# Performance work log

Measured on AMD Instinct MI355X. Metric: run time of the kernel, lower is better.

Reference implementation:

```python
import jax, jax.numpy as jnp
import numpy as np

# --- config (matches init_kwargs) ---
HID = 2048      # hidden_size
H = 16          # num_attention_heads
D_NOPE = 128    # qk_nope_head_dim
D_ROPE = 64     # qk_rope_head_dim
D_Q = D_NOPE + D_ROPE  # 192
D_V = 128       # v_head_dim
QR = 1536       # q_lora_rank
KVR = 512       # kv_lora_rank
PH = 16         # pattern_heads
PD = HID // PH  # 128
THETA = 10000.0
EPS = 1e-6


def rmsnorm(x, w):
    var = jnp.mean(jnp.square(x), axis=-1, keepdims=True)
    return x * jax.lax.rsqrt(var + EPS) * w


def rope_cos_sin(seq_len):
    inv_freq = 1.0 / (THETA ** (jnp.arange(0, D_ROPE, 2, dtype=jnp.float32) / D_ROPE))
    t = jnp.arange(seq_len, dtype=jnp.float32)
    freqs = jnp.outer(t, inv_freq)            # [S, D_ROPE/2]
    emb = jnp.concatenate([freqs, freqs], -1)  # [S, D_ROPE]
    return jnp.cos(emb), jnp.sin(emb)


def rotate_half(x):
    x1, x2 = jnp.split(x, 2, axis=-1)
    return jnp.concatenate([-x2, x1], axis=-1)


def apply_rope(x, cos, sin):
    # x: [B, H, S, D_ROPE]; cos/sin: [S, D_ROPE]
    return x * cos[None, None] + rotate_half(x) * sin[None, None]


def setup_inputs() -> dict:
    key = jax.random.key(0)
    ks = jax.random.split(key, 12)
    def w(k, shape):
        return (jax.random.normal(k, shape, jnp.float32) / np.sqrt(shape[-1])).astype(jnp.float32)
    B, S = 2, 1024
    return {
        "hidden_states": jax.random.normal(ks[0], (B, S, HID), jnp.float32),
        "q_a_w": w(ks[1], (QR, HID)),
        "q_a_ln_w": jnp.ones((QR,), jnp.float32),
        "q_b_w": w(ks[2], (H * D_Q, QR)),
        "kv_a_w": w(ks[3], (KVR + H * D_ROPE, HID)),
        "kv_a_ln_w": jnp.ones((KVR,), jnp.float32),
        "kv_b_w": w(ks[4], (H * (D_NOPE + D_V), KVR)),
        "o_w": w(ks[5], (HID, H * D_V)),
        "sp_q_w": w(ks[6], (HID, HID)),
        "sp_k_w": w(ks[7], (HID, HID)),
        "sp_v_w": w(ks[8], (HID, HID)),
        "sp_o_w": w(ks[9], (HID, HID)),
        "gate_w": w(ks[10], (2, HID)),
        "gate_b": jnp.zeros((2,), jnp.float32),
    }


def reference(hidden_states, q_a_w, q_a_ln_w, q_b_w, kv_a_w, kv_a_ln_w, kv_b_w,
              o_w, sp_q_w, sp_k_w, sp_v_w, sp_o_w, gate_w, gate_b):
    b, s, _ = hidden_states.shape
    dt = hidden_states.dtype

    # ---- main MLA path ----
    q_mid = rmsnorm(hidden_states @ q_a_w.T, q_a_ln_w)                      # [B,S,QR]
    q = (q_mid @ q_b_w.T).reshape(b, s, H, D_Q).transpose(0, 2, 1, 3)       # [B,H,S,Dq]
    q_nope, q_pe = q[..., :D_NOPE], q[..., D_NOPE:]

    kv_a = hidden_states @ kv_a_w.T                                         # [B,S,KVR+H*Dr]
    kv_lora, k_pe_flat = kv_a[..., :KVR], kv_a[..., KVR:]
    k_pe = k_pe_flat.reshape(b, s, H, D_ROPE).transpose(0, 2, 1, 3)         # [B,H,S,Dr]

    kv = (rmsnorm(kv_lora, kv_a_ln_w) @ kv_b_w.T)
    kv = kv.reshape(b, s, H, D_NOPE + D_V).transpose(0, 2, 1, 3)            # [B,H,S,Dn+Dv]
    k_nope, v = kv[..., :D_NOPE], kv[..., D_NOPE:]

    cos, sin = rope_cos_sin(s)
    q_pe = apply_rope(q_pe, cos, sin)
    k_pe = apply_rope(k_pe, cos, sin)

    qf = jnp.concatenate([q_nope, q_pe], -1)                                # [B,H,S,Dq]
    kf = jnp.concatenate([k_nope, k_pe], -1)

    scale = D_Q ** -0.5
    scores = jnp.einsum('bhqd,bhkd->bhqk', qf, kf) * scale
    probs = jax.nn.softmax(scores.astype(jnp.float32), axis=-1).astype(dt)
    ctx = jnp.einsum('bhqk,bhkd->bhqd', probs, v)                           # [B,H,S,Dv]
    main_out = ctx.transpose(0, 2, 1, 3).reshape(b, s, H * D_V) @ o_w.T     # [B,S,HID]

    # ---- self pattern path (standard MHA on hidden_states) ----
    def split_heads(x):
        return x.reshape(b, s, PH, PD).transpose(0, 2, 1, 3)
    pq = split_heads(hidden_states @ sp_q_w.T)
    pk = split_heads(hidden_states @ sp_k_w.T)
    pv = split_heads(hidden_states @ sp_v_w.T)
    p_scores = jnp.einsum('bhqd,bhkd->bhqk', pq, pk) * (PD ** -0.5)
    p_probs = jax.nn.softmax(p_scores.astype(jnp.float32), axis=-1).astype(dt)
    p_ctx = jnp.einsum('bhqk,bhkd->bhqd', p_probs, pv)
    pattern_out = p_ctx.transpose(0, 2, 1, 3).reshape(b, s, HID) @ sp_o_w.T

    # ---- learned gate over paths ----
    gates = jax.nn.softmax(hidden_states @ gate_w.T + gate_b, axis=-1)      # [B,S,2]
    return gates[..., 0:1] * main_out + gates[..., 1:2] * pattern_out
```

## Files before the change

kernel.cpp:

```cpp
#include <hip/hip_runtime.h>
#include <math.h>
#include <stdint.h>

#define HIDN  2048
#define NH    16
#define DNOPE 128
#define DROPE 64
#define DQ    192
#define DV    128
#define QRANK 1536
#define KVRANK 512
#define SEQ   1024
#define NBATCH 2
#define NTOK  (NBATCH*SEQ)
#define EPSV  1e-6f

typedef unsigned short u16;
typedef unsigned int   u32;
typedef __attribute__((ext_vector_type(8))) short  short8;
typedef __attribute__((ext_vector_type(8))) unsigned short ushort8;
typedef __attribute__((ext_vector_type(4))) float  f32x4;

__device__ __forceinline__ u16 f2b(float f) {
    u32 u = __float_as_uint(f);
    u = (u + 0x7fffu + ((u >> 16) & 1u)) >> 16;
    return (u16)u;
}
__device__ __forceinline__ float b2f(u16 h) {
    return __uint_as_float(((u32)h) << 16);
}

__device__ __forceinline__ void async_copy16(const u16* g, u16* l) {
    __builtin_amdgcn_global_load_lds(
        (const __attribute__((address_space(1))) u32*)g,
        (__attribute__((address_space(3))) u32*)l,
        16, 0, 0);
}

__device__ __forceinline__ int swz(int r, int c) { return r * 4 + (c ^ ((r >> 1) & 3)); }

struct CastArgs {
    const float* s[10];
    u16* d[10];
    int cum[11];
};
__global__ __launch_bounds__(256)
void cast_all(CastArgs a, int total_chunks)
{
    int c = blockIdx.x * 256 + threadIdx.x;
    if (c >= total_chunks) return;
    int seg = 0;
    #pragma unroll
    for (int i = 1; i < 10; ++i) seg += (c >= a.cum[i]) ? 1 : 0;
    int local = c - a.cum[seg];
    const float* src = a.s[seg] + (size_t)local * 8;
    u16* dst = a.d[seg] + (size_t)local * 8;
    float4 x = *(const float4*)(src);
    float4 y = *(const float4*)(src + 4);
    ushort8 o;
    o[0]=f2b(x.x); o[1]=f2b(x.y); o[2]=f2b(x.z); o[3]=f2b(x.w);
    o[4]=f2b(y.x); o[5]=f2b(y.y); o[6]=f2b(y.z); o[7]=f2b(y.w);
    *(ushort8*)(dst) = o;
}

struct GemmSeg {
    const u16* X; const u16* W;
    float* Cf; u16* Cb; u16* Cb2; u16* Cb3;
    int K; int ldx; int ldc; int mode; int bx0;
};
struct GemmArgs { GemmSeg seg[3]; int nseg; };

__global__ __launch_bounds__(256)
void gemm_multi(GemmArgs a)
{
    __shared__ __align__(16) u16 As[2 * 4096];
    __shared__ __align__(16) u16 Bs[2 * 4096];
    int s = 0;
    if (a.nseg > 1 && (int)blockIdx.x >= a.seg[1].bx0) s = 1;
    if (a.nseg > 2 && (int)blockIdx.x >= a.seg[2].bx0) s = 2;
    const GemmSeg g = a.seg[s];

    const int tid = threadIdx.x;
    const int bn = ((int)blockIdx.x - g.bx0) * 128;
    const int bm = blockIdx.y * 128;
    const int lane = tid & 63, wv = tid >> 6;
    const int lm = lane & 15, lq = lane >> 4;
    const int wm = (wv >> 1) * 64, wn = (wv & 1) * 64;
    const int ldx = g.ldx, K = g.K;
    const u16* Xp = g.X;
    const u16* Wp = g.W;

    auto stage = [&](int kt, int buf) {
        int k0 = kt * 32;
        #pragma unroll
        for (int it = 0; it < 2; ++it) {
            int base = wv * 64 + it * 256;
            int slot = base + lane;
            int r = slot >> 2, c = (slot & 3) ^ ((r >> 1) & 3);
            async_copy16(Xp + (size_t)(bm + r) * ldx + k0 + c * 8,
                         As + buf * 4096 + base * 8);
            async_copy16(Wp + (size_t)(bn + r) * K + k0 + c * 8,
                         Bs + buf * 4096 + base * 8);
        }
    };

    f32x4 acc[4][4] = {};
    const int niter = K >> 5;
    stage(0, 0);
    for (int kt = 0; kt < niter; ++kt) {
        int cur = kt & 1;
        __syncthreads();
        if (kt + 1 < niter) stage(kt + 1, cur ^ 1);
        const u16* Ab = As + cur * 4096;
        const u16* Bb = Bs + cur * 4096;
        short8 af[4], bf[4];
        #pragma unroll
        for (int mt = 0; mt < 4; ++mt) {
            int R = wm + mt * 16 + lm;
            af[mt] = *(const short8*)(Ab + swz(R, lq) * 8);
        }
        #pragma unroll
        for (int nt = 0; nt < 4; ++nt) {
            int R = wn + nt * 16 + lm;
            bf[nt] = *(const short8*)(Bb + swz(R, lq) * 8);
        }
        #pragma unroll
        for (int mt = 0; mt < 4; ++mt)
            #pragma unroll
            for (int nt = 0; nt < 4; ++nt)
                acc[mt][nt] = __builtin_amdgcn_mfma_f32_16x16x32_bf16(
                    af[mt], bf[nt], acc[mt][nt], 0, 0, 0);
    }

    const int mode = g.mode;
    #pragma unroll
    for (int mt = 0; mt < 4; ++mt) {
        int token0 = bm + wm + mt * 16 + lq * 4;
        #pragma unroll
        for (int nt = 0; nt < 4; ++nt) {
            int feat = bn + wn + nt * 16 + lm;
            #pragma unroll
            for (int i = 0; i < 4; ++i) {
                float v = acc[mt][nt][i];
                int tok = token0 + i;
                int b2 = tok >> 10, s2 = tok & (SEQ - 1);
                if (mode == 0) {
                    g.Cf[(size_t)tok * g.ldc + feat] = v;
                } else if (mode == 5) {
                    g.Cb[(size_t)tok * g.ldc + feat] = f2b(v);
                } else if (mode == 1) {
                    int h2 = feat / DQ, d = feat - h2 * DQ;
                    g.Cb[((size_t)((b2 * NH + h2) * SEQ + s2)) * DQ + d] = f2b(v);
                } else if (mode == 3) {
                    int h2 = feat >> 8, c = feat & 255;
                    if (c < 128)
                        g.Cb[((size_t)((b2 * NH + h2) * SEQ + s2)) * DQ + c] = f2b(v);
                    else
                        g.Cb2[((size_t)((b2 * NH + h2) * 128 + (c - 128))) * SEQ + s2] = f2b(v);
                } else {
                    int wsel = feat >> 11;
                    int f2 = feat & 2047;
                    int h2 = f2 >> 7, d = f2 & 127;
                    if (wsel == 0)
                        g.Cb[((size_t)((b2 * NH + h2) * SEQ + s2)) * 128 + d] = f2b(v);
                    else if (wsel == 1)
                        g.Cb2[((size_t)((b2 * NH + h2) * SEQ + s2)) * 128 + d] = f2b(v);
                    else
                        g.Cb3[((size_t)((b2 * NH + h2) * 128 + d)) * SEQ + s2] = f2b(v);
                }
            }
        }
    }
}

__global__ __launch_bounds__(256)
void rmsnorm_fused(u16* __restrict__ amid, const float* __restrict__ qw,
                   const float* __restrict__ kvw)
{
    int row = blockIdx.x;
    u16* x; const float* w; int D;
    if (row < NTOK) { x = amid + (size_t)row * 3072;            w = qw;  D = QRANK; }
    else            { x = amid + (size_t)(row - NTOK) * 3072 + QRANK; w = kvw; D = KVRANK; }
    float ss = 0.f;
    for (int d = threadIdx.x; d < D; d += 256) { float v = b2f(x[d]); ss += v * v; }
    __shared__ float red[256];
    red[threadIdx.x] = ss;
    __syncthreads();
    for (int off = 128; off > 0; off >>= 1) {
        if (threadIdx.x < off) red[threadIdx.x] += red[threadIdx.x + off];
        __syncthreads();
    }
    float inv = rsqrtf(red[0] / (float)D + EPSV);
    for (int d = threadIdx.x; d < D; d += 256)
        x[d] = f2b(b2f(x[d]) * inv * w[d]);
}

__global__ __launch_bounds__(256)
void rope_fused(u16* __restrict__ qf, const u16* __restrict__ amid,
                u16* __restrict__ kf)
{
    int t = blockIdx.x * 256 + threadIdx.x;
    bool isq = t < (1 << 20);
    int tt = isq ? t : t - (1 << 20);
    int i = tt & 31, s = (tt >> 5) & (SEQ - 1), bh = tt >> 15;
    float inv_freq = exp2f((float)i * -0.41524101186f);
    float ang = (float)s * inv_freq;
    float c, sn; sincosf(ang, &sn, &c);
    if (isq) {
        u16* p = qf + ((size_t)bh * SEQ + s) * DQ;
        float x1 = b2f(p[DNOPE + i]), x2 = b2f(p[DNOPE + 32 + i]);
        p[DNOPE + i]      = f2b(x1 * c - x2 * sn);
        p[DNOPE + 32 + i] = f2b(x2 * c + x1 * sn);
    } else {
        int h = bh & (NH - 1), bb = bh >> 4;
        const u16* src = amid + ((size_t)(bb * SEQ + s)) * 3072 + (QRANK + KVRANK) + h * DROPE;
        float x1 = b2f(src[i]), x2 = b2f(src[32 + i]);
        u16* dst = kf + ((size_t)bh * SEQ + s) * DQ + DNOPE;
        dst[i]      = f2b(x1 * c - x2 * sn);
        dst[32 + i] = f2b(x2 * c + x1 * sn);
    }
}

template<int DQK>
__device__ __forceinline__
void flash_body(const u16* __restrict__ Q, const u16* __restrict__ Kf,
                const u16* __restrict__ Vt, u16* __restrict__ ctx_out,
                float scale, u16* Ks, u16* Vs, u16* Ps, int qt, int h, int bb)
{
    constexpr int KSZ  = 32 * DQK;
    constexpr int VSZ  = 32 * 128;
    constexpr int NKIT = DQK / 64;
    constexpr int NT   = SEQ / 32;
    const int tid = threadIdx.x, lane = tid & 63, wv = tid >> 6;
    const int lm = lane & 15, lq = lane >> 4;
    const size_t bh = (size_t)bb * NH + h;
    const u16* Qb = Q + (bh * SEQ + qt * 64 + wv * 16) * (size_t)DQK;
    const u16* Kb = Kf + bh * SEQ * (size_t)DQK;
    const u16* Vb = Vt + bh * (size_t)128 * SEQ;

    short8 qfrag[DQK / 32];
    #pragma unroll
    for (int ks = 0; ks < DQK / 32; ++ks)
        qfrag[ks] = *(const short8*)(Qb + lm * DQK + ks * 32 + lq * 8);

    auto stage = [&](int kt, int buf) {
        #pragma unroll
        for (int it = 0; it < NKIT; ++it) {
            int base = it * 256 + wv * 64;
            int slot = base + lane;
            int plane = slot >> 7, rem = slot & 127;
            int key = rem >> 2, c = (rem & 3) ^ ((key >> 1) & 3);
            async_copy16(Kb + (size_t)(kt * 32 + key) * DQK + plane * 32 + c * 8,
                         Ks + buf * KSZ + base * 8);
        }
        #pragma unroll
        for (int it = 0; it < 2; ++it) {
            int base = it * 256 + wv * 64;
            int slot = base + lane;
            int d = slot >> 2, c = (slot & 3) ^ ((d >> 1) & 3);
            async_copy16(Vb + (size_t)d * SEQ + kt * 32 + c * 8,
                         Vs + buf * VSZ + base * 8);
        }
    };

    float m_i[4], l_i[4];
    #pragma unroll
    for (int i = 0; i < 4; ++i) { m_i[i] = -INFINITY; l_i[i] = 0.f; }
    f32x4 oacc[8] = {};

    stage(0, 0);
    for (int kt = 0; kt < NT; ++kt) {
        int cur = kt & 1;
        __syncthreads();
        if (kt + 1 < NT) stage(kt + 1, cur ^ 1);
        const u16* Kc = Ks + cur * KSZ;
        const u16* Vc = Vs + cur * VSZ;

        f32x4 sacc[2] = {};
        __builtin_amdgcn_s_setprio(1);
        #pragma unroll
        for (int kb = 0; kb < 2; ++kb)
            #pragma unroll
            for (int ks = 0; ks < DQK / 32; ++ks) {
                int R = kb * 16 + lm;
                short8 kfr = *(const short8*)(Kc + ks * 1024 + swz(R, lq) * 8);
                sacc[kb] = __builtin_amdgcn_mfma_f32_16x16x32_bf16(
                    qfrag[ks], kfr, sacc[kb], 0, 0, 0);
            }
        __builtin_amdgcn_s_setprio(0);

        float s0v[4], s1v[4], mx[4];
        #pragma unroll
        for (int i = 0; i < 4; ++i) {
            float s0 = sacc[0][i] * scale, s1 = sacc[1][i] * scale;
            float m2 = fmaxf(s0, s1);
            m2 = fmaxf(m2, __shfl_xor(m2, 1));
            m2 = fmaxf(m2, __shfl_xor(m2, 2));
            m2 = fmaxf(m2, __shfl_xor(m2, 4));
            m2 = fmaxf(m2, __shfl_xor(m2, 8));
            s0v[i] = s0; s1v[i] = s1; mx[i] = m2;
        }
        bool need = false;
        #pragma unroll
        for (int i = 0; i < 4; ++i) need |= (mx[i] > m_i[i] + 8.f);
        need = __any(need);
        float alpha[4];
        if (need) {
            #pragma unroll
            for (int i = 0; i < 4; ++i) {
                float mnew = fmaxf(m_i[i], mx[i]);
                alpha[i] = __expf(m_i[i] - mnew);
                m_i[i] = mnew;
                l_i[i] *= alpha[i];
            }
        }
        float p0[4], p1[4];
        #pragma unroll
        for (int i = 0; i < 4; ++i) {
            p0[i] = __expf(s0v[i] - m_i[i]);
            p1[i] = __expf(s1v[i] - m_i[i]);
            float sum = p0[i] + p1[i];
            sum += __shfl_xor(sum, 1);
            sum += __shfl_xor(sum, 2);
            sum += __shfl_xor(sum, 4);
            sum += __shfl_xor(sum, 8);
            l_i[i] += sum;
        }

        u16* Pw = Ps + wv * 640;
        #pragma unroll
        for (int i = 0; i < 4; ++i) {
            Pw[(lq * 4 + i) * 40 + lm]      = f2b(p0[i]);
            Pw[(lq * 4 + i) * 40 + 16 + lm] = f2b(p1[i]);
        }
        short8 pfrag = *(const short8*)(Pw + lm * 40 + lq * 8);

        if (need) {
            #pragma unroll
            for (int nt = 0; nt < 8; ++nt)
                #pragma unroll
                for (int i = 0; i < 4; ++i) oacc[nt][i] *= alpha[i];
        }
        __builtin_amdgcn_s_setprio(1);
        #pragma unroll
        for (int nt = 0; nt < 8; ++nt) {
            int R = nt * 16 + lm;
            short8 vfr = *(const short8*)(Vc + swz(R, lq) * 8);
            oacc[nt] = __builtin_amdgcn_mfma_f32_16x16x32_bf16(
                pfrag, vfr, oacc[nt], 0, 0, 0);
        }
        __builtin_amdgcn_s_setprio(0);
    }

    int s0 = qt * 64 + wv * 16 + lq * 4;
    #pragma unroll
    for (int i = 0; i < 4; ++i) {
        float inv = 1.f / l_i[i];
        u16* dst = ctx_out + ((size_t)(bb * SEQ + s0 + i) * NH + h) * 128;
        #pragma unroll
        for (int nt = 0; nt < 8; ++nt)
            dst[nt * 16 + lm] = f2b(oacc[nt][i] * inv);
    }
}

__global__ __launch_bounds__(256, 3)
void flash_fused(const u16* qf, const u16* kf, const u16* Vtg, u16* ctx,
                 const u16* pq, const u16* pk, const u16* pvt, u16* p_ctx,
                 float scale_main, float scale_pat)
{
    __shared__ __align__(16) u16 Ks[2 * 32 * DQ];
    __shared__ __align__(16) u16 Vs[2 * 32 * 128];
    __shared__ __align__(16) u16 Ps[4 * 16 * 40];
    int h = blockIdx.x, qtb = blockIdx.y, bb = blockIdx.z;
    if (qtb < 16)
        flash_body<DQ>(qf, kf, Vtg, ctx, scale_main, Ks, Vs, Ps, qtb, h, bb);
    else
        flash_body<128>(pq, pk, pvt, p_ctx, scale_pat, Ks, Vs, Ps, qtb - 16, h, bb);
}

__global__ __launch_bounds__(256)
void gate_combine(const float* __restrict__ x, const float* __restrict__ gw,
                  const float* __restrict__ gb,
                  const float* __restrict__ mo, const float* __restrict__ po,
                  float* __restrict__ out)
{
    const int tok = blockIdx.x;
    const float* xr = x + (size_t)tok * HIDN;
    float d0 = 0.f, d1 = 0.f;
    for (int i = threadIdx.x; i < HIDN; i += 256) {
        float v = xr[i];
        d0 += v * gw[i];
        d1 += v * gw[HIDN + i];
    }
    __shared__ float r0[256], r1[256];
    r0[threadIdx.x] = d0; r1[threadIdx.x] = d1;
    __syncthreads();
    for (int off = 128; off > 0; off >>= 1) {
        if (threadIdx.x < off) {
            r0[threadIdx.x] += r0[threadIdx.x + off];
            r1[threadIdx.x] += r1[threadIdx.x + off];
        }
        __syncthreads();
    }
    float l0 = r0[0] + gb[0], l1 = r1[0] + gb[1];
    float m = fmaxf(l0, l1);
    float e0 = __expf(l0 - m), e1 = __expf(l1 - m);
    float g0 = e0 / (e0 + e1), g1 = e1 / (e0 + e1);
    const float* mr = mo + (size_t)tok * HIDN;
    const float* pr = po + (size_t)tok * HIDN;
    float* orow = out + (size_t)tok * HIDN;
    for (int i = threadIdx.x; i < HIDN; i += 256)
        orow[i] = g0 * mr[i] + g1 * pr[i];
}

extern "C" void kernel_launch(void* const* d_in, const int* in_sizes, int n_in,
                              void* d_out, int out_size, void* d_ws, size_t ws_size,
                              hipStream_t stream)
{
    const float* X        = (const float*)d_in[0];
    const float* q_a_w    = (const float*)d_in[1];
    const float* q_a_ln_w = (const float*)d_in[2];
    const float* q_b_w    = (const float*)d_in[3];
    const float* kv_a_w   = (const float*)d_in[4];
    const float* kv_a_ln_w= (const float*)d_in[5];
    const float* kv_b_w   = (const float*)d_in[6];
    const float* o_w      = (const float*)d_in[7];
    const float* sp_q_w   = (const float*)d_in[8];
    const float* sp_k_w   = (const float*)d_in[9];
    const float* sp_v_w   = (const float*)d_in[10];
    const float* sp_o_w   = (const float*)d_in[11];
    const float* gate_w   = (const float*)d_in[12];
    const float* gate_b   = (const float*)d_in[13];
    float* out = (float*)d_out;

    char* p = (char*)d_ws;
    auto alloc = [&](size_t bytes) -> char* {
        char* r = p; p += (bytes + 255) & ~(size_t)255; return r;
    };
    u16* amid      = (u16*)alloc((size_t)NTOK * 3072 * 2);
    u16* Xb        = (u16*)alloc((size_t)NTOK * HIDN * 2);
    u16* aw_b      = (u16*)alloc((size_t)3072 * HIDN * 2);
    u16* q_b_wb    = (u16*)alloc((size_t)NH * DQ * QRANK * 2);
    u16* kv_b_wb   = (u16*)alloc((size_t)NH * 256 * KVRANK * 2);
    u16* o_wb      = (u16*)alloc((size_t)HIDN * HIDN * 2);
    u16* spqkv_wb  = (u16*)alloc((size_t)3 * HIDN * HIDN * 2);
    u16* sp_o_wb   = (u16*)alloc((size_t)HIDN * HIDN * 2);
    u16* qf        = (u16*)alloc((size_t)NTOK * NH * DQ * 2);
    u16* kf        = (u16*)alloc((size_t)NTOK * NH * DQ * 2);
    u16* Vtg       = (u16*)alloc((size_t)NBATCH * NH * 128 * SEQ * 2);
    u16* pq        = (u16*)alloc((size_t)NTOK * HIDN * 2);
    u16* pk        = (u16*)alloc((size_t)NTOK * HIDN * 2);
    u16* pvt    = aw_b;
    u16* ctx    = q_b_wb;
    u16* p_ctx  = spqkv_wb;
    float* patout = (float*)qf;

    dim3 blk(256);

    CastArgs ca;
    const float* srcs[10] = {X, q_a_w, kv_a_w, q_b_w, kv_b_w, o_w,
                             sp_q_w, sp_k_w, sp_v_w, sp_o_w};
    u16* dsts[10] = {Xb, aw_b, aw_b + (size_t)QRANK * HIDN, q_b_wb, kv_b_wb, o_wb,
                     spqkv_wb, spqkv_wb + (size_t)HIDN * HIDN,
                     spqkv_wb + (size_t)2 * HIDN * HIDN, sp_o_wb};
    int ns[10] = {NTOK * HIDN, QRANK * HIDN, 1536 * HIDN, NH * DQ * QRANK,
                  NH * 256 * KVRANK, HIDN * HIDN, HIDN * HIDN, HIDN * HIDN,
                  HIDN * HIDN, HIDN * HIDN};
    int cum = 0;
    for (int i = 0; i < 10; ++i) {
        ca.s[i] = srcs[i]; ca.d[i] = dsts[i];
        ca.cum[i] = cum; cum += ns[i] / 8;
    }
    ca.cum[10] = cum;
    cast_all<<<dim3((cum + 255) / 256), blk, 0, stream>>>(ca, cum);

    {
        GemmArgs ga = {};
        ga.nseg = 1;
        ga.seg[0] = {Xb, aw_b, nullptr, amid, nullptr, nullptr,
                     HIDN, HIDN, 3072, 5, 0};
        gemm_multi<<<dim3(24, 16), blk, 0, stream>>>(ga);
    }

    rmsnorm_fused<<<dim3(2 * NTOK), blk, 0, stream>>>(amid, q_a_ln_w, kv_a_ln_w);

    {
        GemmArgs ga = {};
        ga.nseg = 3;
        ga.seg[0] = {Xb, spqkv_wb, nullptr, pq, pk, pvt,
                     HIDN, HIDN, 0, 4, 0};
        ga.seg[1] = {amid, q_b_wb, nullptr, qf, nullptr, nullptr,
                     QRANK, 3072, 0, 1, 48};
        ga.seg[2] = {amid + QRANK, kv_b_wb, nullptr, kf, Vtg, nullptr,
                     KVRANK, 3072, 0, 3, 72};
        gemm_multi<<<dim3(104, 16), blk, 0, stream>>>(ga);
    }

    rope_fused<<<dim3(8192), blk, 0, stream>>>(qf, amid, kf);

    flash_fused<<<dim3(NH, 32, NBATCH), blk, 0, stream>>>(
        qf, kf, Vtg, ctx, pq, pk, pvt, p_ctx,
        1.0f / sqrtf((float)DQ), 1.0f / sqrtf(128.0f));

    {
        GemmArgs ga = {};
        ga.nseg = 2;
        ga.seg[0] = {ctx, o_wb, out, nullptr, nullptr, nullptr,
                     HIDN, HIDN, HIDN, 0, 0};
        ga.seg[1] = {p_ctx, sp_o_wb, patout, nullptr, nullptr, nullptr,
                     HIDN, HIDN, HIDN, 0, 16};
        gemm_multi<<<dim3(32, 16), blk, 0, stream>>>(ga);
    }

    gate_combine<<<dim3(NTOK), blk, 0, stream>>>(X, gate_w, gate_b, out, patout, out);
}
```

Baseline: 598.9 us.

## Process 32 query rows per wave in flash attention to reuse K/V fragments

Each wave now handles two 16-row query sub-tiles (128 queries per block instead of 64), so every K and V fragment loaded from LDS feeds two MFMAs. This halves the grid, halves K/V global staging per query, and drops the setprio hints and the occupancy target from 3 to 2 blocks. The cost is doubled accumulator and softmax-state registers, lower occupancy and fewer blocks (512) to spread across CUs.

```diff
diff --git a/kernel.cpp b/kernel.cpp
--- a/kernel.cpp
+++ b/kernel.cpp
@@ -234,14 +234,16 @@
     const int tid = threadIdx.x, lane = tid & 63, wv = tid >> 6;
     const int lm = lane & 15, lq = lane >> 4;
     const size_t bh = (size_t)bb * NH + h;
-    const u16* Qb = Q + (bh * SEQ + qt * 64 + wv * 16) * (size_t)DQK;
+    const u16* Qb = Q + (bh * SEQ + qt * 128 + wv * 32) * (size_t)DQK;
     const u16* Kb = Kf + bh * SEQ * (size_t)DQK;
     const u16* Vb = Vt + bh * (size_t)128 * SEQ;
 
-    short8 qfrag[DQK / 32];
+    short8 qfrag[2][DQK / 32];
     #pragma unroll
-    for (int ks = 0; ks < DQK / 32; ++ks)
-        qfrag[ks] = *(const short8*)(Qb + lm * DQK + ks * 32 + lq * 8);
+    for (int rh = 0; rh < 2; ++rh)
+        #pragma unroll
+        for (int ks = 0; ks < DQK / 32; ++ks)
+            qfrag[rh][ks] = *(const short8*)(Qb + (rh * 16 + lm) * DQK + ks * 32 + lq * 8);
 
     auto stage = [&](int kt, int buf) {
         #pragma unroll
@@ -263,10 +265,12 @@
         }
     };
 
-    float m_i[4], l_i[4];
+    float m_i[2][4], l_i[2][4];
     #pragma unroll
-    for (int i = 0; i < 4; ++i) { m_i[i] = -INFINITY; l_i[i] = 0.f; }
-    f32x4 oacc[8] = {};
+    for (int rh = 0; rh < 2; ++rh)
+        #pragma unroll
+        for (int i = 0; i < 4; ++i) { m_i[rh][i] = -INFINITY; l_i[rh][i] = 0.f; }
+    f32x4 oacc[2][8] = {};
 
     stage(0, 0);
     for (int kt = 0; kt < NT; ++kt) {
@@ -276,106 +280,118 @@
         const u16* Kc = Ks + cur * KSZ;
         const u16* Vc = Vs + cur * VSZ;
 
-        f32x4 sacc[2] = {};
-        __builtin_amdgcn_s_setprio(1);
+        f32x4 sacc[2][2] = {};
         #pragma unroll
         for (int kb = 0; kb < 2; ++kb)
             #pragma unroll
             for (int ks = 0; ks < DQK / 32; ++ks) {
                 int R = kb * 16 + lm;
                 short8 kfr = *(const short8*)(Kc + ks * 1024 + swz(R, lq) * 8);
-                sacc[kb] = __builtin_amdgcn_mfma_f32_16x16x32_bf16(
-                    qfrag[ks], kfr, sacc[kb], 0, 0, 0);
+                sacc[0][kb] = __builtin_amdgcn_mfma_f32_16x16x32_bf16(
+                    qfrag[0][ks], kfr, sacc[0][kb], 0, 0, 0);
+                sacc[1][kb] = __builtin_amdgcn_mfma_f32_16x16x32_bf16(
+                    qfrag[1][ks], kfr, sacc[1][kb], 0, 0, 0);
             }
-        __builtin_amdgcn_s_setprio(0);
-
-        float s0v[4], s1v[4], mx[4];
-        #pragma unroll
-        for (int i = 0; i < 4; ++i) {
-            float s0 = sacc[0][i] * scale, s1 = sacc[1][i] * scale;
-            float m2 = fmaxf(s0, s1);
-            m2 = fmaxf(m2, __shfl_xor(m2, 1));
-            m2 = fmaxf(m2, __shfl_xor(m2, 2));
-            m2 = fmaxf(m2, __shfl_xor(m2, 4));
-            m2 = fmaxf(m2, __shfl_xor(m2, 8));
-            s0v[i] = s0; s1v[i] = s1; mx[i] = m2;
-        }
-        bool need = false;
-        #pragma unroll
-        for (int i = 0; i < 4; ++i) need |= (mx[i] > m_i[i] + 8.f);
-        need = __any(need);
-        float alpha[4];
+
+        float p0[2][4], p1[2][4], mx[2][4];
+        bool needb = false;
+        #pragma unroll
+        for (int rh = 0; rh < 2; ++rh)
+            #pragma unroll
+            for (int i = 0; i < 4; ++i) {
+                float s0 = sacc[rh][0][i] * scale, s1 = sacc[rh][1][i] * scale;
+                float m2 = fmaxf(s0, s1);
+                m2 = fmaxf(m2, __shfl_xor(m2, 1));
+                m2 = fmaxf(m2, __shfl_xor(m2, 2));
+                m2 = fmaxf(m2, __shfl_xor(m2, 4));
+                m2 = fmaxf(m2, __shfl_xor(m2, 8));
+                p0[rh][i] = s0; p1[rh][i] = s1; mx[rh][i] = m2;
+                needb |= (m2 > m_i[rh][i] + 8.f);
+            }
+        bool need = __any(needb);
+        float alpha[2][4];
         if (need) {
             #pragma unroll
+            for (int rh = 0; rh < 2; ++rh)
+                #pragma unroll
+                for (int i = 0; i < 4; ++i) {
+                    float mnew = fmaxf(m_i[rh][i], mx[rh][i]);
+                    alpha[rh][i] = __expf(m_i[rh][i] - mnew);
+                    m_i[rh][i] = mnew;
+                    l_i[rh][i] *= alpha[rh][i];
+                }
+        }
+        #pragma unroll
+        for (int rh = 0; rh < 2; ++rh)
+            #pragma unroll
             for (int i = 0; i < 4; ++i) {
-                float mnew = fmaxf(m_i[i], mx[i]);
-                alpha[i] = __expf(m_i[i] - mnew);
-                m_i[i] = mnew;
-                l_i[i] *= alpha[i];
+                p0[rh][i] = __expf(p0[rh][i] - m_i[rh][i]);
+                p1[rh][i] = __expf(p1[rh][i] - m_i[rh][i]);
+                float sum = p0[rh][i] + p1[rh][i];
+                sum += __shfl_xor(sum, 1);
+                sum += __shfl_xor(sum, 2);
+                sum += __shfl_xor(sum, 4);
+                sum += __shfl_xor(sum, 8);
+                l_i[rh][i] += sum;
             }
-        }
-        float p0[4], p1[4];
-        #pragma unroll
-        for (int i = 0; i < 4; ++i) {
-            p0[i] = __expf(s0v[i] - m_i[i]);
-            p1[i] = __expf(s1v[i] - m_i[i]);
-            float sum = p0[i] + p1[i];
-            sum += __shfl_xor(sum, 1);
-            sum += __shfl_xor(sum, 2);
-            sum += __shfl_xor(sum, 4);
-            sum += __shfl_xor(sum, 8);
-            l_i[i] += sum;
-        }
-
-        u16* Pw = Ps + wv * 640;
-        #pragma unroll
-        for (int i = 0; i < 4; ++i) {
-            Pw[(lq * 4 + i) * 40 + lm]      = f2b(p0[i]);
-            Pw[(lq * 4 + i) * 40 + 16 + lm] = f2b(p1[i]);
-        }
-        short8 pfrag = *(const short8*)(Pw + lm * 40 + lq * 8);
+
+        u16* Pw = Ps + wv * 1280;
+        #pragma unroll
+        for (int rh = 0; rh < 2; ++rh)
+            #pragma unroll
+            for (int i = 0; i < 4; ++i) {
+                Pw[(rh * 16 + lq * 4 + i) * 40 + lm]      = f2b(p0[rh][i]);
+                Pw[(rh * 16 + lq * 4 + i) * 40 + 16 + lm] = f2b(p1[rh][i]);
+            }
+        short8 pfrag0 = *(const short8*)(Pw + lm * 40 + lq * 8);
+        short8 pfrag1 = *(const short8*)(Pw + (16 + lm) * 40 + lq * 8);
 
         if (need) {
             #pragma unroll
-            for (int nt = 0; nt < 8; ++nt)
+            for (int rh = 0; rh < 2; ++rh)
                 #pragma unroll
-                for (int i = 0; i < 4; ++i) oacc[nt][i] *= alpha[i];
-        }
-        __builtin_amdgcn_s_setprio(1);
+                for (int nt = 0; nt < 8; ++nt)
+                    #pragma unroll
+                    for (int i = 0; i < 4; ++i) oacc[rh][nt][i] *= alpha[rh][i];
+        }
         #pragma unroll
         for (int nt = 0; nt < 8; ++nt) {
             int R = nt * 16 + lm;
             short8 vfr = *(const short8*)(Vc + swz(R, lq) * 8);
-            oacc[nt] = __builtin_amdgcn_mfma_f32_16x16x32_bf16(
-                pfrag, vfr, oacc[nt], 0, 0, 0);
-        }
-        __builtin_amdgcn_s_setprio(0);
-    }
-
-    int s0 = qt * 64 + wv * 16 + lq * 4;
+            oacc[0][nt] = __builtin_amdgcn_mfma_f32_16x16x32_bf16(
+                pfrag0, vfr, oacc[0][nt], 0, 0, 0);
+            oacc[1][nt] = __builtin_amdgcn_mfma_f32_16x16x32_bf16(
+                pfrag1, vfr, oacc[1][nt], 0, 0, 0);
+        }
+    }
+
     #pragma unroll
-    for (int i = 0; i < 4; ++i) {
-        float inv = 1.f / l_i[i];
-        u16* dst = ctx_out + ((size_t)(bb * SEQ + s0 + i) * NH + h) * 128;
-        #pragma unroll
-        for (int nt = 0; nt < 8; ++nt)
-            dst[nt * 16 + lm] = f2b(oacc[nt][i] * inv);
-    }
-}
-
-__global__ __launch_bounds__(256, 3)
+    for (int rh = 0; rh < 2; ++rh) {
+        int s0 = qt * 128 + wv * 32 + rh * 16 + lq * 4;
+        #pragma unroll
+        for (int i = 0; i < 4; ++i) {
+            float inv = 1.f / l_i[rh][i];
+            u16* dst = ctx_out + ((size_t)(bb * SEQ + s0 + i) * NH + h) * 128;
+            #pragma unroll
+            for (int nt = 0; nt < 8; ++nt)
+                dst[nt * 16 + lm] = f2b(oacc[rh][nt][i] * inv);
+        }
+    }
+}
+
+__global__ __launch_bounds__(256, 2)
 void flash_fused(const u16* qf, const u16* kf, const u16* Vtg, u16* ctx,
                  const u16* pq, const u16* pk, const u16* pvt, u16* p_ctx,
                  float scale_main, float scale_pat)
 {
     __shared__ __align__(16) u16 Ks[2 * 32 * DQ];
     __shared__ __align__(16) u16 Vs[2 * 32 * 128];
-    __shared__ __align__(16) u16 Ps[4 * 16 * 40];
+    __shared__ __align__(16) u16 Ps[4 * 32 * 40];
     int h = blockIdx.x, qtb = blockIdx.y, bb = blockIdx.z;
-    if (qtb < 16)
+    if (qtb < 8)
         flash_body<DQ>(qf, kf, Vtg, ctx, scale_main, Ks, Vs, Ps, qtb, h, bb);
     else
-        flash_body<128>(pq, pk, pvt, p_ctx, scale_pat, Ks, Vs, Ps, qtb - 16, h, bb);
+        flash_body<128>(pq, pk, pvt, p_ctx, scale_pat, Ks, Vs, Ps, qtb - 8, h, bb);
 }
 
 __global__ __launch_bounds__(256)
@@ -498,7 +514,7 @@
 
     rope_fused<<<dim3(8192), blk, 0, stream>>>(qf, amid, kf);
 
-    flash_fused<<<dim3(NH, 32, NBATCH), blk, 0, stream>>>(
+    flash_fused<<<dim3(NH, 16, NBATCH), blk, 0, stream>>>(
         qf, kf, Vtg, ctx, pq, pk, pvt, p_ctx,
         1.0f / sqrtf((float)DQ), 1.0f / sqrtf(128.0f));
 
```

New measurement: 585.8 us. -2.2%, faster.
